# Kernel optimization log

Hardware: AMD Instinct MI355X
Metric: run time of the kernel (lower is better)

Reference implementation:

```python
import jax, jax.numpy as jnp
import numpy as np
import math

B, T, D = 1, 2048, 1024          # batch, seq, d_model
H, HS = 16, 64                    # heads, head_size
E, K, L = 8, 2, 2                 # experts, top_k, layers
V = 32000                         # llama tokenizer vocab
CAP = (B * T * K) // E            # expert capacity = 512
HALF = HS // 2


def _layernorm(x, w, b):
    m = jnp.mean(x, -1, keepdims=True)
    v = jnp.var(x, -1, keepdims=True)
    return (x - m) / jnp.sqrt(v + 1e-5) * w + b


def _rope_sincos():
    pos = jnp.arange(T, dtype=jnp.float32)[:, None]
    div = jnp.exp(jnp.arange(0, HALF * 2, 2, dtype=jnp.float32) * (-math.log(10000.0) / (HALF * 2)))
    return jnp.sin(pos * div), jnp.cos(pos * div)


def _attention(x, qkv_w, out_w, sin, cos):
    qkv = (x @ qkv_w.T).reshape(B, T, 3, H, HS)
    q, k, v = qkv[:, :, 0], qkv[:, :, 1], qkv[:, :, 2]
    s_, c_ = sin[None, :, None, :], cos[None, :, None, :]

    def rot(t):
        t1, t2 = t[..., :HALF], t[..., HALF:]
        return jnp.concatenate([t1 * c_ - t2 * s_, t2 * c_ + t1 * s_], -1)

    q, k = rot(q), rot(k)
    scores = jnp.einsum('bthd,bshd->bhts', q, k) / math.sqrt(HS)
    mask = jnp.tril(jnp.ones((T, T), bool))
    scores = jnp.where(mask[None, None], scores, -1e30)
    p = jax.nn.softmax(scores, -1)
    av = jnp.einsum('bhts,bshd->bthd', p, v)  # [B,T,H,HS]
    # faithful to torch source: permute(0,2,1,3).reshape(B,T,C)
    return av.transpose(0, 2, 1, 3).reshape(B, T, D) @ out_w.T


def _moe(x, noise_l, rw, rb, nw, nb, w1, b1, w2, b2):
    # NoisyTopkRouter + capacity-limited dispatch / expert MLP / weighted combine
    N = B * T
    xf = x.reshape(N, D)
    logits = xf @ rw.T + rb
    noisy = logits + noise_l.reshape(N, E) * jax.nn.softplus(xf @ nw.T + nb)
    topv, topi = jax.lax.top_k(noisy, K)
    # softmax over sparse logits (-inf elsewhere) == softmax over top-k values
    gate = jax.nn.softmax(topv, -1).reshape(-1)  # [N*K]
    ef = topi.reshape(-1)                        # expert id per (token,k) pair
    tid = jnp.repeat(jnp.arange(N), K)           # token id per pair
    oh = jax.nn.one_hot(ef, E, dtype=jnp.int32)
    # position of this token in its expert's arrival order (token-major, as nonzero())
    rank = (jnp.cumsum(oh, 0) - oh)[jnp.arange(N * K), ef]
    valid = rank < CAP
    pos = jnp.where(valid, ef * CAP + rank, E * CAP)  # dummy slot for dropped tokens
    disp = jnp.zeros((E * CAP + 1, D), x.dtype).at[pos].set(xf[tid])
    de = disp[:E * CAP].reshape(E, CAP, D)
    h = jax.nn.relu(jnp.einsum('ecd,efd->ecf', de, w1) + b1[:, None, :])
    eo = jnp.einsum('ecf,edf->ecd', h, w2) + b2[:, None, :]
    eo = jnp.concatenate([eo.reshape(E * CAP, D), jnp.zeros((1, D), x.dtype)], 0)
    contrib = eo[pos] * (gate * valid.astype(x.dtype))[:, None]
    return jax.ops.segment_sum(contrib, tid, num_segments=N).reshape(B, T, D)


def _forward(input_ids, noise, tok_emb, pos_emb, ln1_w, ln1_b, ln2_w, ln2_b,
             qkv_w, out_w, router_w, router_b, noise_w, noise_b,
             e_w1, e_b1, e_w2, e_b2, lnf_w, lnf_b):
    sin, cos = _rope_sincos()
    x = tok_emb[input_ids] + pos_emb[:T]
    for l in range(L):
        x = x + _attention(_layernorm(x, ln1_w[l], ln1_b[l]), qkv_w[l], out_w[l], sin, cos)
        x = x + _moe(_layernorm(x, ln2_w[l], ln2_b[l]), noise[l],
                     router_w[l], router_b[l], noise_w[l], noise_b[l],
                     e_w1[l], e_b1[l], e_w2[l], e_b2[l])
    return _layernorm(x, lnf_w, lnf_b)


def setup_inputs() -> dict:
    key = jax.random.key(0)
    ks = jax.random.split(key, 16)
    s = 0.02
    inp = {
        'input_ids': jax.random.randint(ks[0], (B, T), 0, V),
        'noise': jax.random.normal(ks[1], (L, B, T, E), jnp.float32),
        'tok_emb': jax.random.normal(ks[2], (V, D), jnp.float32) * s,
        'pos_emb': jax.random.normal(ks[3], (T, D), jnp.float32) * s,
        'ln1_w': jnp.ones((L, D), jnp.float32), 'ln1_b': jnp.zeros((L, D), jnp.float32),
        'ln2_w': jnp.ones((L, D), jnp.float32), 'ln2_b': jnp.zeros((L, D), jnp.float32),
        'qkv_w': jax.random.normal(ks[4], (L, 3 * D, D), jnp.float32) * s,
        'out_w': jax.random.normal(ks[5], (L, D, D), jnp.float32) * s,
        'router_w': jax.random.normal(ks[6], (L, E, D), jnp.float32) * s,
        'router_b': jnp.zeros((L, E), jnp.float32),
        'noise_w': jax.random.normal(ks[7], (L, E, D), jnp.float32) * s,
        'noise_b': jnp.zeros((L, E), jnp.float32),
        'e_w1': jax.random.normal(ks[8], (L, E, 4 * D, D), jnp.float32) * s,
        'e_b1': jnp.zeros((L, E, 4 * D), jnp.float32),
        'e_w2': jax.random.normal(ks[9], (L, E, D, 4 * D), jnp.float32) * s,
        'e_b2': jnp.zeros((L, E, D), jnp.float32),
        'lnf_w': jnp.ones((D,), jnp.float32), 'lnf_b': jnp.zeros((D,), jnp.float32),
    }
    return inp


def reference(input_ids, noise, tok_emb, pos_emb, ln1_w, ln1_b, ln2_w, ln2_b,
              qkv_w, out_w, router_w, router_b, noise_w, noise_b,
              e_w1, e_b1, e_w2, e_b2, lnf_w, lnf_b):
    return _forward(input_ids, noise, tok_emb, pos_emb, ln1_w, ln1_b, ln2_w, ln2_b,
                    qkv_w, out_w, router_w, router_b, noise_w, noise_b,
                    e_w1, e_b1, e_w2, e_b2, lnf_w, lnf_b)
```

## Files before the change

### kernel.cpp

```cpp
#include <hip/hip_runtime.h>
#include <math.h>

#define TT   2048
#define DD   1024
#define HH   16
#define HSS  64
#define EE   8
#define KTOP 2
#define LL   2
#define CAPP 512
#define NN   2048
#define DFF  4096
#define NK   (NN*KTOP)
#define HALF 32

typedef __attribute__((ext_vector_type(8))) short bf16x8;
typedef __attribute__((ext_vector_type(4))) float f32x4;

__device__ __forceinline__ void split3(float v, short& s0, short& s1, short& s2) {
  union { float f; unsigned u; } a, b0, c, b1, d;
  a.f = v;
  unsigned t0 = (a.u + 0x7fffu + ((a.u >> 16) & 1u)) & 0xffff0000u;
  b0.u = t0;
  float r1 = v - b0.f;
  c.f = r1;
  unsigned t1 = (c.u + 0x7fffu + ((c.u >> 16) & 1u)) & 0xffff0000u;
  b1.u = t1;
  float r2 = r1 - b1.f;
  d.f = r2;
  unsigned t2 = d.u + 0x7fffu + ((d.u >> 16) & 1u);
  s0 = (short)(t0 >> 16); s1 = (short)(t1 >> 16); s2 = (short)(t2 >> 16);
}

__device__ __forceinline__ void gld16(const short* g, short* l) {
  __builtin_amdgcn_global_load_lds(
      (const __attribute__((address_space(1))) unsigned int*)g,
      (__attribute__((address_space(3))) unsigned int*)l, 16, 0, 0);
}

__global__ __launch_bounds__(256) void embed_kernel(const int* __restrict__ ids,
                                                    const float* __restrict__ tok,
                                                    const float* __restrict__ pos,
                                                    float* __restrict__ x) {
  int t = blockIdx.x, tid = threadIdx.x;
  int id = ids[t];
  float4 a = ((const float4*)(tok + (long long)id * DD))[tid];
  float4 b = ((const float4*)(pos + (long long)t * DD))[tid];
  float4 r;
  r.x = a.x + b.x; r.y = a.y + b.y; r.z = a.z + b.z; r.w = a.w + b.w;
  ((float4*)(x + (long long)t * DD))[tid] = r;
}

__global__ __launch_bounds__(256) void sincos_kernel(float* __restrict__ st, float* __restrict__ ct) {
  int idx = blockIdx.x * 256 + threadIdx.x;
  int t = idx >> 5, i = idx & 31;
  double div = exp(-(double)(2 * i) * (9.210340371976184 / 64.0));
  double a = (double)t * div;
  st[idx] = (float)sin(a);
  ct[idx] = (float)cos(a);
}

__global__ __launch_bounds__(256) void convert_kernel(const float* __restrict__ in,
                                                      short* __restrict__ out, long long n) {
  long long i = ((long long)blockIdx.x * 256 + threadIdx.x) * 8;
  float4 v0 = *(const float4*)(in + i);
  float4 v1 = *(const float4*)(in + i + 4);
  float vv[8] = {v0.x, v0.y, v0.z, v0.w, v1.x, v1.y, v1.z, v1.w};
  short s0[8], s1[8], s2[8];
#pragma unroll
  for (int j = 0; j < 8; j++) split3(vv[j], s0[j], s1[j], s2[j]);
  *(short4*)(out + i)         = make_short4(s0[0], s0[1], s0[2], s0[3]);
  *(short4*)(out + i + 4)     = make_short4(s0[4], s0[5], s0[6], s0[7]);
  *(short4*)(out + n + i)     = make_short4(s1[0], s1[1], s1[2], s1[3]);
  *(short4*)(out + n + i + 4) = make_short4(s1[4], s1[5], s1[6], s1[7]);
  *(short4*)(out + 2*n + i)   = make_short4(s2[0], s2[1], s2[2], s2[3]);
  *(short4*)(out + 2*n + i+4) = make_short4(s2[4], s2[5], s2[6], s2[7]);
}

__global__ __launch_bounds__(256) void ln_kernel(const float* __restrict__ in, float* __restrict__ out,
                                                 short* __restrict__ yp,
                                                 const float* __restrict__ w, const float* __restrict__ b) {
  int row = blockIdx.x, tid = threadIdx.x;
  float4 v = ((const float4*)(in + (long long)row * DD))[tid];
  float s = v.x + v.y + v.z + v.w;
  float q = v.x * v.x + v.y * v.y + v.z * v.z + v.w * v.w;
#pragma unroll
  for (int off = 32; off > 0; off >>= 1) {
    s += __shfl_down(s, off);
    q += __shfl_down(q, off);
  }
  __shared__ float rs[4], rq[4];
  int wv = tid >> 6;
  if ((tid & 63) == 0) { rs[wv] = s; rq[wv] = q; }
  __syncthreads();
  float S = rs[0] + rs[1] + rs[2] + rs[3];
  float Q = rq[0] + rq[1] + rq[2] + rq[3];
  float mean = S * (1.0f / DD);
  float var = Q * (1.0f / DD) - mean * mean;
  float rstd = rsqrtf(var + 1e-5f);
  float4 wv4 = ((const float4*)w)[tid];
  float4 bv4 = ((const float4*)b)[tid];
  float4 r;
  r.x = (v.x - mean) * rstd * wv4.x + bv4.x;
  r.y = (v.y - mean) * rstd * wv4.y + bv4.y;
  r.z = (v.z - mean) * rstd * wv4.z + bv4.z;
  r.w = (v.w - mean) * rstd * wv4.w + bv4.w;
  ((float4*)(out + (long long)row * DD))[tid] = r;
  if (yp) {
    float rr[4] = {r.x, r.y, r.z, r.w};
    short a0[4], a1[4], a2[4];
#pragma unroll
    for (int j = 0; j < 4; j++) split3(rr[j], a0[j], a1[j], a2[j]);
    size_t off = (size_t)row * DD + tid * 4;
    *(short4*)(yp + off)                    = make_short4(a0[0], a0[1], a0[2], a0[3]);
    *(short4*)(yp + (size_t)NN*DD + off)    = make_short4(a1[0], a1[1], a1[2], a1[3]);
    *(short4*)(yp + (size_t)2*NN*DD + off)  = make_short4(a2[0], a2[1], a2[2], a2[3]);
  }
}

__global__ __launch_bounds__(256) void gemm_kernel(
    const float* __restrict__ Aall, const float* __restrict__ Ball,
    const float* __restrict__ biasAll, const float* __restrict__ resAll,
    float* __restrict__ Call, int M, int Nn, int Kd, int flags,
    long long sA, long long sB, long long sBias, long long sC) {
  const float* A = Aall + (long long)blockIdx.z * sA;
  const float* B = Ball + (long long)blockIdx.z * sB;
  float* C = Call + (long long)blockIdx.z * sC;
  __shared__ float As[128 * 17];
  __shared__ float Bs[128 * 17];
  int tid = threadIdx.x;
  int tx = tid & 15, ty = tid >> 4;
  int bm = blockIdx.y * 128, bn = blockIdx.x * 128;
  int lrow = tid >> 2;
  int lk = (tid & 3) << 2;
  float acc[8][8];
#pragma unroll
  for (int i = 0; i < 8; i++)
#pragma unroll
    for (int j = 0; j < 8; j++) acc[i][j] = 0.f;
  const float* Arow0 = A + (long long)(bm + lrow) * Kd + lk;
  const float* Arow1 = A + (long long)(bm + lrow + 64) * Kd + lk;
  const float* Brow0 = B + (long long)(bn + lrow) * Kd + lk;
  const float* Brow1 = B + (long long)(bn + lrow + 64) * Kd + lk;
  for (int kb = 0; kb < Kd; kb += 16) {
    float4 a0 = *(const float4*)(Arow0 + kb);
    float4 a1 = *(const float4*)(Arow1 + kb);
    float4 b0 = *(const float4*)(Brow0 + kb);
    float4 b1 = *(const float4*)(Brow1 + kb);
    __syncthreads();
    As[lrow * 17 + lk + 0] = a0.x; As[lrow * 17 + lk + 1] = a0.y;
    As[lrow * 17 + lk + 2] = a0.z; As[lrow * 17 + lk + 3] = a0.w;
    As[(lrow + 64) * 17 + lk + 0] = a1.x; As[(lrow + 64) * 17 + lk + 1] = a1.y;
    As[(lrow + 64) * 17 + lk + 2] = a1.z; As[(lrow + 64) * 17 + lk + 3] = a1.w;
    Bs[lrow * 17 + lk + 0] = b0.x; Bs[lrow * 17 + lk + 1] = b0.y;
    Bs[lrow * 17 + lk + 2] = b0.z; Bs[lrow * 17 + lk + 3] = b0.w;
    Bs[(lrow + 64) * 17 + lk + 0] = b1.x; Bs[(lrow + 64) * 17 + lk + 1] = b1.y;
    Bs[(lrow + 64) * 17 + lk + 2] = b1.z; Bs[(lrow + 64) * 17 + lk + 3] = b1.w;
    __syncthreads();
#pragma unroll
    for (int k = 0; k < 16; k++) {
      float av[8], bv[8];
#pragma unroll
      for (int i = 0; i < 8; i++) av[i] = As[(ty + 16 * i) * 17 + k];
#pragma unroll
      for (int j = 0; j < 8; j++) bv[j] = Bs[(tx + 16 * j) * 17 + k];
#pragma unroll
      for (int i = 0; i < 8; i++)
#pragma unroll
        for (int j = 0; j < 8; j++) acc[i][j] = fmaf(av[i], bv[j], acc[i][j]);
    }
  }
  const float* bias = (flags & 1) ? (biasAll + (long long)blockIdx.z * sBias) : nullptr;
  const float* res = (flags & 4) ? (resAll + (long long)blockIdx.z * sC) : nullptr;
#pragma unroll
  for (int i = 0; i < 8; i++) {
    int row = bm + ty + 16 * i;
#pragma unroll
    for (int j = 0; j < 8; j++) {
      int col = bn + tx + 16 * j;
      float v = acc[i][j];
      if (flags & 1) v += bias[col];
      if (flags & 2) v = fmaxf(v, 0.f);
      if (flags & 4) v += res[(long long)row * Nn + col];
      C[(long long)row * Nn + col] = v;
    }
  }
}

__global__ __launch_bounds__(256, 3) void gemm_mfma(
    const short* __restrict__ Ap, const short* __restrict__ Bp,
    const float* __restrict__ biasAll, const float* __restrict__ resAll,
    void* __restrict__ Call, int M, int Nn, int Kd, int flags,
    long long sA, long long sB, long long sBias, long long sC,
    long long PA, long long PB, long long PC) {
  const bool fast = (flags & 8);
  const int np = fast ? 2 : 3;
  const int splitK = (flags >> 8) & 0xff;
  __shared__ short As[3][128][32];
  __shared__ short Bs[3][128][32];
  int tid = threadIdx.x;

  int gx = gridDim.x, gy = gridDim.y;
  int nwg = gx * gy * gridDim.z;
  int flat = blockIdx.x + gx * (blockIdx.y + gy * blockIdx.z);
  int cpx = nwg >> 3;
  int wkid = (flat & 7) * cpx + (flat >> 3);
  int bz = wkid / (gx * gy);
  int rem = wkid - bz * gx * gy;
  int by = rem / gx, bx = rem - by * gx;

  int sk = 0, e = bz, kLen = Kd;
  if (splitK > 1) { sk = bz % splitK; e = bz / splitK; kLen = Kd / splitK; }
  int k0 = sk * kLen;

  int bm = by * 128, bn = bx * 128;
  long long zA = (long long)e * sA;
  long long zB = (long long)e * sB;

  int wid = tid >> 6, lane = tid & 63;
  int lrow = lane >> 2, lchunk = lane & 3;
  int cs = lchunk ^ ((lrow >> 1) & 3);
  const short* gAbase = Ap + zA + (long long)(bm + wid * 16 + lrow) * Kd + cs * 8;
  const short* gBbase = Bp + zB + (long long)(bn + wid * 16 + lrow) * Kd + cs * 8;
  long long hstepA = (long long)64 * Kd;

  int wm = (wid & 1) * 64, wn = (wid >> 1) * 64;
  int tr = lane & 15, quad = lane >> 4;
  int qsw = (quad ^ ((tr >> 1) & 3)) << 3;

  f32x4 acc[4][4];
#pragma unroll
  for (int i = 0; i < 4; i++)
#pragma unroll
    for (int j = 0; j < 4; j++) acc[i][j] = (f32x4){0.f, 0.f, 0.f, 0.f};

  for (int kb = k0; kb < k0 + kLen; kb += 32) {
    __syncthreads();
#pragma unroll
    for (int p = 0; p < 3; p++) {
      if (p < np) {
#pragma unroll
        for (int h = 0; h < 2; h++) {
          int rb = h * 64 + wid * 16;
          gld16(gAbase + p * PA + h * hstepA + kb, &As[p][rb][0]);
          gld16(gBbase + p * PB + h * hstepA + kb, &Bs[p][rb][0]);
        }
      }
    }
    __syncthreads();
    bf16x8 af[4][3];
#pragma unroll
    for (int mi = 0; mi < 4; mi++) {
      int ar = wm + mi * 16 + tr;
      af[mi][0] = *(const bf16x8*)&As[0][ar][qsw];
      af[mi][1] = *(const bf16x8*)&As[1][ar][qsw];
      af[mi][2] = fast ? af[mi][0] : *(const bf16x8*)&As[2][ar][qsw];
    }
#pragma unroll
    for (int nj = 0; nj < 4; nj++) {
      int br = wn + nj * 16 + tr;
      bf16x8 b0 = *(const bf16x8*)&Bs[0][br][qsw];
      bf16x8 b1 = *(const bf16x8*)&Bs[1][br][qsw];
      bf16x8 b2 = fast ? b0 : *(const bf16x8*)&Bs[2][br][qsw];
#pragma unroll
      for (int mi = 0; mi < 4; mi++) {
        f32x4 c = acc[mi][nj];
        c = __builtin_amdgcn_mfma_f32_16x16x32_bf16(af[mi][1], b0, c, 0, 0, 0);
        c = __builtin_amdgcn_mfma_f32_16x16x32_bf16(af[mi][0], b1, c, 0, 0, 0);
        if (!fast) {
          c = __builtin_amdgcn_mfma_f32_16x16x32_bf16(af[mi][2], b0, c, 0, 0, 0);
          c = __builtin_amdgcn_mfma_f32_16x16x32_bf16(af[mi][1], b1, c, 0, 0, 0);
          c = __builtin_amdgcn_mfma_f32_16x16x32_bf16(af[mi][0], b2, c, 0, 0, 0);
        }
        c = __builtin_amdgcn_mfma_f32_16x16x32_bf16(af[mi][0], b0, c, 0, 0, 0);
        acc[mi][nj] = c;
      }
    }
  }

  long long z = e;
  if (splitK > 1) {
    int NB = nwg / (gx * gy) / splitK;
    float* P = (float*)Call;
    long long base = ((long long)sk * NB + e) * sC;
#pragma unroll
    for (int mi = 0; mi < 4; mi++)
#pragma unroll
      for (int nj = 0; nj < 4; nj++) {
        int col = bn + wn + nj * 16 + tr;
#pragma unroll
        for (int rg = 0; rg < 4; rg++) {
          int row = bm + wm + mi * 16 + quad * 4 + rg;
          P[base + (long long)row * Nn + col] = acc[mi][nj][rg];
        }
      }
    return;
  }
  const float* bias = (flags & 1) ? (biasAll + z * sBias) : nullptr;
  if (flags & 16) {
    short* Cs = (short*)Call;
#pragma unroll
    for (int mi = 0; mi < 4; mi++)
#pragma unroll
      for (int nj = 0; nj < 4; nj++) {
        int col = bn + wn + nj * 16 + tr;
#pragma unroll
        for (int rg = 0; rg < 4; rg++) {
          int row = bm + wm + mi * 16 + quad * 4 + rg;
          float v = acc[mi][nj][rg];
          if (flags & 1) v += bias[col];
          if (flags & 2) v = fmaxf(v, 0.f);
          short s0, s1, s2;
          split3(v, s0, s1, s2);
          long long off = z * sC + (long long)row * Nn + col;
          Cs[off] = s0; Cs[PC + off] = s1; Cs[2 * PC + off] = s2;
        }
      }
  } else {
    float* C = (float*)Call;
    const float* res = (flags & 4) ? (resAll + z * sC) : nullptr;
#pragma unroll
    for (int mi = 0; mi < 4; mi++)
#pragma unroll
      for (int nj = 0; nj < 4; nj++) {
        int col = bn + wn + nj * 16 + tr;
#pragma unroll
        for (int rg = 0; rg < 4; rg++) {
          int row = bm + wm + mi * 16 + quad * 4 + rg;
          float v = acc[mi][nj][rg];
          if (flags & 1) v += bias[col];
          if (flags & 2) v = fmaxf(v, 0.f);
          if (flags & 4) v += res[(long long)row * Nn + col];
          C[z * sC + (long long)row * Nn + col] = v;
        }
      }
  }
  (void)M;
}

__global__ __launch_bounds__(256) void reduce_kernel(
    float* __restrict__ dst, const float* __restrict__ part,
    const float* __restrict__ biasAll, int splits, long long total,
    int Nn, long long MNn, long long sBias, int flags) {
  long long i = ((long long)blockIdx.x * 256 + threadIdx.x) * 4;
  if (i >= total) return;
  float4 v = make_float4(0.f, 0.f, 0.f, 0.f);
  for (int s = 0; s < splits; s++) {
    float4 p = *(const float4*)(part + (long long)s * total + i);
    v.x += p.x; v.y += p.y; v.z += p.z; v.w += p.w;
  }
  if (flags & 1) {
    long long e = i / MNn;
    int col = (int)(i % Nn);
    const float* b = biasAll + e * sBias + col;
    v.x += b[0]; v.y += b[1]; v.z += b[2]; v.w += b[3];
  }
  if (flags & 4) {
    float4 r = *(const float4*)(dst + i);
    v.x += r.x; v.y += r.y; v.z += r.z; v.w += r.w;
  }
  *(float4*)(dst + i) = v;
}

__global__ __launch_bounds__(256) void rope_kernel(float* __restrict__ qkv,
                                                   const float* __restrict__ st,
                                                   const float* __restrict__ ct) {
  int t = blockIdx.x, tid = threadIdx.x;
#pragma unroll
  for (int p = tid; p < HH * HALF; p += 256) {
    int h = p >> 5, i = p & 31;
    float s = st[t * HALF + i], c = ct[t * HALF + i];
    float* q = qkv + (long long)t * (3 * DD) + h * HSS;
    float q1 = q[i], q2 = q[i + HALF];
    q[i] = q1 * c - q2 * s;
    q[i + HALF] = q2 * c + q1 * s;
    float* k = q + DD;
    float k1 = k[i], k2 = k[i + HALF];
    k[i] = k1 * c - k2 * s;
    k[i + HALF] = k2 * c + k1 * s;
  }
}

__global__ __launch_bounds__(256, 1) void attn_kernel(const float* __restrict__ qkv,
                                                      float* __restrict__ attn,
                                                      short* __restrict__ ap) {
  int bid = blockIdx.x;
  int head = bid & 15;
  int qc = (bid < 256) ? (31 - (bid >> 4)) : ((bid - 256) >> 4);
  int tid = threadIdx.x;
  int w = tid >> 6;
  int r = tid & 63;
  int qrow = qc * 64 + r;
  int nkt = qc + 1;

  __shared__ float4 KVbuf[4][2][16][16];
  __shared__ float Ms[4][64];
  __shared__ float Ls[4][64];

  float4 q[16], o[16];
  const float4* qp = (const float4*)(qkv + (long long)qrow * (3 * DD) + head * HSS);
#pragma unroll
  for (int d = 0; d < 16; d++) { q[d] = qp[d]; o[d] = make_float4(0.f, 0.f, 0.f, 0.f); }
  float m = -INFINITY, l = 0.f;

  for (int kt = w; kt < nkt; kt += 4) {
    bool diag = (kt == qc);
#pragma unroll 1
    for (int s = 0; s < 4; s++) {
      int kbase = kt * 64 + s * 16;
#pragma unroll
      for (int it = 0; it < 4; it++) {
        int fid = r + it * 64;
        int krow = fid >> 4, d4 = fid & 15;
        const float* bK = qkv + (long long)(kbase + krow) * (3 * DD) + DD + head * HSS + d4 * 4;
        KVbuf[w][0][krow][d4] = *(const float4*)bK;
        KVbuf[w][1][krow][d4] = *(const float4*)(bK + DD);
      }
      float sbuf[16];
#pragma unroll
      for (int jj = 0; jj < 16; jj++) {
        const float4* kr = KVbuf[w][0][jj];
        float sv = 0.f;
#pragma unroll
        for (int d = 0; d < 16; d++) {
          float4 kv = kr[d];
          sv = fmaf(q[d].x, kv.x, sv); sv = fmaf(q[d].y, kv.y, sv);
          sv = fmaf(q[d].z, kv.z, sv); sv = fmaf(q[d].w, kv.w, sv);
        }
        sv *= 0.125f;
        if (diag && (kbase + jj > qrow)) sv = -1e30f;
        sbuf[jj] = sv;
      }
      float gm = m;
#pragma unroll
      for (int jj = 0; jj < 16; jj++) gm = fmaxf(gm, sbuf[jj]);
      float scale = __expf(m - gm);
      m = gm;
      l *= scale;
#pragma unroll
      for (int d = 0; d < 16; d++) {
        o[d].x *= scale; o[d].y *= scale; o[d].z *= scale; o[d].w *= scale;
      }
#pragma unroll
      for (int jj = 0; jj < 16; jj++) {
        float p = __expf(sbuf[jj] - m);
        l += p;
        const float4* vr = KVbuf[w][1][jj];
#pragma unroll
        for (int d = 0; d < 16; d++) {
          float4 vv = vr[d];
          o[d].x = fmaf(p, vv.x, o[d].x); o[d].y = fmaf(p, vv.y, o[d].y);
          o[d].z = fmaf(p, vv.z, o[d].z); o[d].w = fmaf(p, vv.w, o[d].w);
        }
      }
    }
  }

  typedef float4 OscRow[64][5];
  OscRow* Osc = reinterpret_cast<OscRow*>(&KVbuf[0][0][0][0]);
  int rr = tid & 63, ii = tid >> 6;
  long long obase = (long long)head * TT * HSS + (long long)(qc * 64 + rr) * HSS;
#pragma unroll
  for (int c = 0; c < 4; c++) {
    __syncthreads();
    Osc[w][r][0] = o[c * 4 + 0];
    Osc[w][r][1] = o[c * 4 + 1];
    Osc[w][r][2] = o[c * 4 + 2];
    Osc[w][r][3] = o[c * 4 + 3];
    if (c == 0) { Ms[w][r] = m; Ls[w][r] = l; }
    __syncthreads();
    float m0 = Ms[0][rr], m1 = Ms[1][rr], m2 = Ms[2][rr], m3 = Ms[3][rr];
    float M = fmaxf(fmaxf(m0, m1), fmaxf(m2, m3));
    float s0 = __expf(m0 - M), s1 = __expf(m1 - M);
    float s2 = __expf(m2 - M), s3 = __expf(m3 - M);
    float L = s0 * Ls[0][rr] + s1 * Ls[1][rr] + s2 * Ls[2][rr] + s3 * Ls[3][rr];
    float rl = 1.f / L;
    float4 a0 = Osc[0][rr][ii], a1 = Osc[1][rr][ii];
    float4 a2 = Osc[2][rr][ii], a3 = Osc[3][rr][ii];
    float4 res;
    res.x = (s0 * a0.x + s1 * a1.x + s2 * a2.x + s3 * a3.x) * rl;
    res.y = (s0 * a0.y + s1 * a1.y + s2 * a2.y + s3 * a3.y) * rl;
    res.z = (s0 * a0.z + s1 * a1.z + s2 * a2.z + s3 * a3.z) * rl;
    res.w = (s0 * a0.w + s1 * a1.w + s2 * a2.w + s3 * a3.w) * rl;
    long long oaddr = obase + c * 16 + ii * 4;
    *(float4*)(attn + oaddr) = res;
    if (ap) {
      float rv[4] = {res.x, res.y, res.z, res.w};
      short p0[4], p1[4], p2[4];
#pragma unroll
      for (int j = 0; j < 4; j++) split3(rv[j], p0[j], p1[j], p2[j]);
      *(short4*)(ap + oaddr)                    = make_short4(p0[0], p0[1], p0[2], p0[3]);
      *(short4*)(ap + (size_t)NN*DD + oaddr)    = make_short4(p1[0], p1[1], p1[2], p1[3]);
      *(short4*)(ap + (size_t)2*NN*DD + oaddr)  = make_short4(p2[0], p2[1], p2[2], p2[3]);
    }
  }
}

__global__ __launch_bounds__(64) void router_kernel(
    const float* __restrict__ y, const float* __restrict__ rw, const float* __restrict__ rb,
    const float* __restrict__ nw, const float* __restrict__ nb, const float* __restrict__ noise,
    int* __restrict__ slot_e, float* __restrict__ slot_g) {
  int n = blockIdx.x;
  int lane = threadIdx.x;
  double accr[EE], accn[EE];
#pragma unroll
  for (int e = 0; e < EE; e++) { accr[e] = 0.0; accn[e] = 0.0; }
  for (int j = 0; j < 16; j++) {
    float xv = y[(long long)n * DD + j * 64 + lane];
#pragma unroll
    for (int e = 0; e < EE; e++) {
      accr[e] += (double)xv * (double)rw[e * DD + j * 64 + lane];
      accn[e] += (double)xv * (double)nw[e * DD + j * 64 + lane];
    }
  }
#pragma unroll
  for (int e = 0; e < EE; e++) {
    for (int off = 32; off > 0; off >>= 1) {
      accr[e] += __shfl_down(accr[e], off);
      accn[e] += __shfl_down(accn[e], off);
    }
  }
  if (lane == 0) {
    float noisy[EE];
#pragma unroll
    for (int e = 0; e < EE; e++) {
      float lg = (float)accr[e] + rb[e];
      float nl = (float)accn[e] + nb[e];
      float sp = (nl > 0.f) ? (nl + log1pf(expf(-nl))) : log1pf(expf(nl));
      noisy[e] = lg + noise[n * EE + e] * sp;
    }
    int i0 = 0;
#pragma unroll
    for (int e = 1; e < EE; e++) if (noisy[e] > noisy[i0]) i0 = e;
    int i1 = -1;
#pragma unroll
    for (int e = 0; e < EE; e++) {
      if (e == i0) continue;
      if (i1 < 0 || noisy[e] > noisy[i1]) i1 = e;
    }
    float v0 = noisy[i0], v1 = noisy[i1];
    float e1 = __expf(v1 - v0);
    float inv = 1.f / (1.f + e1);
    slot_e[2 * n] = i0; slot_e[2 * n + 1] = i1;
    slot_g[2 * n] = inv; slot_g[2 * n + 1] = e1 * inv;
  }
}

__global__ __launch_bounds__(256) void scan_kernel(const int* __restrict__ slot_e,
                                                   int* __restrict__ slot_pos) {
  __shared__ int cnt[256 * EE];
  int tid = threadIdx.x;
  int base = tid * 16;
  int c[EE];
#pragma unroll
  for (int e = 0; e < EE; e++) c[e] = 0;
  int loc[16];
  for (int i = 0; i < 16; i++) {
    int e = slot_e[base + i];
    loc[i] = e;
    c[e]++;
  }
#pragma unroll
  for (int e = 0; e < EE; e++) cnt[tid * EE + e] = c[e];
  __syncthreads();
  if (tid < EE) {
    int run = 0;
    for (int t2 = 0; t2 < 256; t2++) {
      int v = cnt[t2 * EE + tid];
      cnt[t2 * EE + tid] = run;
      run += v;
    }
  }
  __syncthreads();
  int run[EE];
#pragma unroll
  for (int e = 0; e < EE; e++) run[e] = cnt[tid * EE + e];
  for (int i = 0; i < 16; i++) {
    int e = loc[i];
    int r = run[e]++;
    slot_pos[base + i] = (r < CAPP) ? (e * CAPP + r) : -1;
  }
}

__global__ __launch_bounds__(256) void dispatch_kernel(const float* __restrict__ y,
                                                       const int* __restrict__ slot_pos,
                                                       float* __restrict__ disp) {
  int i = blockIdx.x;
  int pos = slot_pos[i];
  if (pos < 0) return;
  int tok = i >> 1;
  ((float4*)(disp + (long long)pos * DD))[threadIdx.x] =
      ((const float4*)(y + (long long)tok * DD))[threadIdx.x];
}

__global__ __launch_bounds__(256) void dispatch_planes_kernel(const short* __restrict__ yp,
                                                              const int* __restrict__ slot_pos,
                                                              short* __restrict__ dp) {
  int i = blockIdx.x;
  int pos = slot_pos[i];
  if (pos < 0) return;
  int tok = i >> 1;
#pragma unroll
  for (int p = 0; p < 3; p++) {
    short4 v = ((const short4*)(yp + (size_t)p * NN * DD + (size_t)tok * DD))[threadIdx.x];
    ((short4*)(dp + (size_t)p * EE * CAPP * DD + (size_t)pos * DD))[threadIdx.x] = v;
  }
}

__global__ __launch_bounds__(256) void combine_kernel(float* __restrict__ x,
                                                      const float* __restrict__ eo,
                                                      const int* __restrict__ slot_pos,
                                                      const float* __restrict__ slot_g) {
  int n = blockIdx.x, tid = threadIdx.x;
  int p0 = slot_pos[2 * n], p1 = slot_pos[2 * n + 1];
  float g0 = slot_g[2 * n], g1 = slot_g[2 * n + 1];
  float4 v = ((float4*)(x + (long long)n * DD))[tid];
  if (p0 >= 0) {
    float4 e0 = ((const float4*)(eo + (long long)p0 * DD))[tid];
    v.x = fmaf(g0, e0.x, v.x); v.y = fmaf(g0, e0.y, v.y);
    v.z = fmaf(g0, e0.z, v.z); v.w = fmaf(g0, e0.w, v.w);
  }
  if (p1 >= 0) {
    float4 e1 = ((const float4*)(eo + (long long)p1 * DD))[tid];
    v.x = fmaf(g1, e1.x, v.x); v.y = fmaf(g1, e1.y, v.y);
    v.z = fmaf(g1, e1.z, v.z); v.w = fmaf(g1, e1.w, v.w);
  }
  ((float4*)(x + (long long)n * DD))[tid] = v;
}

extern "C" void kernel_launch(void* const* d_in, const int* in_sizes, int n_in,
                              void* d_out, int out_size, void* d_ws, size_t ws_size,
                              hipStream_t stream) {
  const int* input_ids = (const int*)d_in[0];
  const float* noise = (const float*)d_in[1];
  const float* tok_emb = (const float*)d_in[2];
  const float* pos_emb = (const float*)d_in[3];
  const float* ln1_w = (const float*)d_in[4];
  const float* ln1_b = (const float*)d_in[5];
  const float* ln2_w = (const float*)d_in[6];
  const float* ln2_b = (const float*)d_in[7];
  const float* qkv_w = (const float*)d_in[8];
  const float* out_w = (const float*)d_in[9];
  const float* router_w = (const float*)d_in[10];
  const float* router_b = (const float*)d_in[11];
  const float* noise_w = (const float*)d_in[12];
  const float* noise_b = (const float*)d_in[13];
  const float* e_w1 = (const float*)d_in[14];
  const float* e_b1 = (const float*)d_in[15];
  const float* e_w2 = (const float*)d_in[16];
  const float* e_b2 = (const float*)d_in[17];
  const float* lnf_w = (const float*)d_in[18];
  const float* lnf_b = (const float*)d_in[19];
  float* out = (float*)d_out;

  float* ws = (float*)d_ws;
  size_t off = 0;
  float* x = ws + off;       off += (size_t)NN * DD;
  float* y = ws + off;       off += (size_t)NN * DD;
  float* qkv = ws + off;     off += (size_t)NN * 3 * DD;
  float* eo = ws + off;      off += (size_t)EE * CAPP * DD;
  float* sintab = ws + off;  off += (size_t)TT * HALF;
  float* costab = ws + off;  off += (size_t)TT * HALF;
  float* attn32 = ws + off;  off += (size_t)NN * DD;
  int* slot_e = (int*)(ws + off);   off += NK;
  int* slot_pos = (int*)(ws + off); off += NK;
  float* slot_g = ws + off;  off += NK;
  size_t base_floats = off;
  float* disp32 = ws + off;
  float* hbuf32 = disp32 + (size_t)EE * CAPP * DD;
  size_t fb_need = (base_floats + (size_t)EE * CAPP * DD + (size_t)EE * CAPP * DFF) * 4;

  short* sp = (short*)(ws + base_floats);
  short* y_p = sp;                                   sp += (size_t)3 * NN * DD;
  short* attn_p = sp;                                sp += (size_t)3 * NN * DD;
  short* disp_p = sp;                                sp += (size_t)3 * EE * CAPP * DD;
  short* hbuf_p = sp;                                sp += (size_t)3 * EE * CAPP * DFF;
  short* qkvw_p = sp;                                sp += (size_t)3 * LL * 3 * DD * DD;
  short* outw_p = sp;                                sp += (size_t)3 * LL * DD * DD;
  short* ew_p = sp;                                  sp += (size_t)3 * EE * DFF * DD;
  size_t mfma_need = (size_t)((char*)sp - (char*)d_ws);
  bool use_mfma = (ws_size >= mfma_need);
  (void)fb_need;

  float* pQKV = (float*)hbuf_p;
  float* pAO  = (float*)hbuf_p;
  float* pM2  = y;

  embed_kernel<<<TT, 256, 0, stream>>>(input_ids, tok_emb, pos_emb, x);
  sincos_kernel<<<(TT * HALF) / 256, 256, 0, stream>>>(sintab, costab);

  if (use_mfma) {
    long long nq = (long long)LL * 3 * DD * DD;
    long long no = (long long)LL * DD * DD;
    convert_kernel<<<(int)(nq / 2048), 256, 0, stream>>>(qkv_w, qkvw_p, nq);
    convert_kernel<<<(int)(no / 2048), 256, 0, stream>>>(out_w, outw_p, no);
    long long ne = (long long)EE * DFF * DD;

    for (int l = 0; l < LL; l++) {
      int fastf = (l == LL - 1) ? 8 : 0;
      ln_kernel<<<NN, 256, 0, stream>>>(x, y, y_p, ln1_w + l * DD, ln1_b + l * DD);
      gemm_mfma<<<dim3(3 * DD / 128, NN / 128, 2), 256, 0, stream>>>(
          y_p, qkvw_p + (size_t)l * 3 * DD * DD, nullptr, nullptr, pQKV,
          NN, 3 * DD, DD, (2 << 8), 0, 0, 0, (long long)NN * 3 * DD,
          (long long)NN * DD, (long long)LL * 3 * DD * DD, 0);
      reduce_kernel<<<(int)((long long)NN * 3 * DD / 1024), 256, 0, stream>>>(
          qkv, pQKV, nullptr, 2, (long long)NN * 3 * DD, 3 * DD,
          (long long)NN * 3 * DD, 0, 0);
      rope_kernel<<<TT, 256, 0, stream>>>(qkv, sintab, costab);
      attn_kernel<<<512, 256, 0, stream>>>(qkv, attn32, attn_p);
      gemm_mfma<<<dim3(DD / 128, NN / 128, 4), 256, 0, stream>>>(
          attn_p, outw_p + (size_t)l * DD * DD, nullptr, nullptr, pAO,
          NN, DD, DD, (4 << 8), 0, 0, 0, (long long)NN * DD,
          (long long)NN * DD, (long long)LL * DD * DD, 0);
      reduce_kernel<<<(int)((long long)NN * DD / 1024), 256, 0, stream>>>(
          x, pAO, nullptr, 4, (long long)NN * DD, DD, (long long)NN * DD, 0, 4);
      ln_kernel<<<NN, 256, 0, stream>>>(x, y, y_p, ln2_w + l * DD, ln2_b + l * DD);
      router_kernel<<<NN, 64, 0, stream>>>(
          y, router_w + (size_t)l * EE * DD, router_b + l * EE,
          noise_w + (size_t)l * EE * DD, noise_b + l * EE,
          noise + (size_t)l * NN * EE, slot_e, slot_g);
      scan_kernel<<<1, 256, 0, stream>>>(slot_e, slot_pos);
      dispatch_planes_kernel<<<NK, 256, 0, stream>>>(y_p, slot_pos, disp_p);
      convert_kernel<<<(int)(ne / 2048), 256, 0, stream>>>(e_w1 + (size_t)l * ne, ew_p, ne);
      gemm_mfma<<<dim3(DFF / 128, CAPP / 128, EE), 256, 0, stream>>>(
          disp_p, ew_p, e_b1 + (size_t)l * EE * DFF, nullptr, hbuf_p,
          CAPP, DFF, DD, 1 | 2 | 16 | fastf,
          (long long)CAPP * DD, (long long)DFF * DD, DFF, (long long)CAPP * DFF,
          (long long)EE * CAPP * DD, (long long)EE * DFF * DD, (long long)EE * CAPP * DFF);
      convert_kernel<<<(int)(ne / 2048), 256, 0, stream>>>(e_w2 + (size_t)l * ne, ew_p, ne);
      gemm_mfma<<<dim3(DD / 128, CAPP / 128, EE * 2), 256, 0, stream>>>(
          hbuf_p, ew_p, nullptr, nullptr, pM2,
          CAPP, DD, DFF, fastf | (2 << 8),
          (long long)CAPP * DFF, (long long)DD * DFF, 0, (long long)CAPP * DD,
          (long long)EE * CAPP * DFF, (long long)EE * DD * DFF, 0);
      reduce_kernel<<<(int)((long long)EE * CAPP * DD / 1024), 256, 0, stream>>>(
          eo, pM2, e_b2 + (size_t)l * EE * DD, 2, (long long)EE * CAPP * DD, DD,
          (long long)CAPP * DD, DD, 1);
      combine_kernel<<<NN, 256, 0, stream>>>(x, eo, slot_pos, slot_g);
    }
  } else {
    for (int l = 0; l < LL; l++) {
      ln_kernel<<<NN, 256, 0, stream>>>(x, y, nullptr, ln1_w + l * DD, ln1_b + l * DD);
      gemm_kernel<<<dim3(3 * DD / 128, NN / 128, 1), 256, 0, stream>>>(
          y, qkv_w + (size_t)l * 3 * DD * DD, nullptr, nullptr, qkv,
          NN, 3 * DD, DD, 0, 0, 0, 0, 0);
      rope_kernel<<<TT, 256, 0, stream>>>(qkv, sintab, costab);
      attn_kernel<<<512, 256, 0, stream>>>(qkv, attn32, nullptr);
      gemm_kernel<<<dim3(DD / 128, NN / 128, 1), 256, 0, stream>>>(
          attn32, out_w + (size_t)l * DD * DD, nullptr, x, x,
          NN, DD, DD, 4, 0, 0, 0, 0);
      ln_kernel<<<NN, 256, 0, stream>>>(x, y, nullptr, ln2_w + l * DD, ln2_b + l * DD);
      router_kernel<<<NN, 64, 0, stream>>>(
          y, router_w + (size_t)l * EE * DD, router_b + l * EE,
          noise_w + (size_t)l * EE * DD, noise_b + l * EE,
          noise + (size_t)l * NN * EE, slot_e, slot_g);
      scan_kernel<<<1, 256, 0, stream>>>(slot_e, slot_pos);
      dispatch_kernel<<<NK, 256, 0, stream>>>(y, slot_pos, disp32);
      gemm_kernel<<<dim3(DFF / 128, CAPP / 128, EE), 256, 0, stream>>>(
          disp32, e_w1 + (size_t)l * EE * DFF * DD, e_b1 + (size_t)l * EE * DFF, nullptr, hbuf32,
          CAPP, DFF, DD, 3,
          (long long)CAPP * DD, (long long)DFF * DD, DFF, (long long)CAPP * DFF);
      gemm_kernel<<<dim3(DD / 128, CAPP / 128, EE), 256, 0, stream>>>(
          hbuf32, e_w2 + (size_t)l * EE * DD * DFF, e_b2 + (size_t)l * EE * DD, nullptr, eo,
          CAPP, DD, DFF, 1,
          (long long)CAPP * DFF, (long long)DD * DFF, DD, (long long)CAPP * DD);
      combine_kernel<<<NN, 256, 0, stream>>>(x, eo, slot_pos, slot_g);
    }
  }
  ln_kernel<<<NN, 256, 0, stream>>>(x, out, nullptr, lnf_w, lnf_b);
  (void)in_sizes; (void)n_in; (void)out_size; (void)ws_size;
}
```

Baseline: 2.559 ms.

## Move causal attention onto bf16 MFMA with split-precision Q/K/V planes

Replaces the fp32 scalar flash-attention kernel with an MFMA-based kernel that uses 3-term bf16 split products (hi*hi, hi*lo, lo*hi) for QK^T and PV. Two new prep kernels fuse RoPE into producing hi/lo bf16 planes for Q and K and write a transposed V in hi/lo planes, staged in LDS through swizzled global_load_lds. The goal is to cut the attention compute cost by using matrix cores, at the price of extra prep passes, workspace traffic and slightly reduced precision versus full fp32.

```diff
diff --git a/kernel.cpp b/kernel.cpp
--- a/kernel.cpp
+++ b/kernel.cpp
@@ -30,6 +30,17 @@
   d.f = r2;
   unsigned t2 = d.u + 0x7fffu + ((d.u >> 16) & 1u);
   s0 = (short)(t0 >> 16); s1 = (short)(t1 >> 16); s2 = (short)(t2 >> 16);
+}
+
+__device__ __forceinline__ void split2(float v, short& s0, short& s1) {
+  union { float f; unsigned u; } a, b0, c;
+  a.f = v;
+  unsigned t0 = (a.u + 0x7fffu + ((a.u >> 16) & 1u)) & 0xffff0000u;
+  b0.u = t0;
+  float r1 = v - b0.f;
+  c.f = r1;
+  unsigned t1 = c.u + 0x7fffu + ((c.u >> 16) & 1u);
+  s0 = (short)(t0 >> 16); s1 = (short)(t1 >> 16);
 }
 
 __device__ __forceinline__ void gld16(const short* g, short* l) {
@@ -381,6 +392,223 @@
   }
 }
 
+__global__ __launch_bounds__(256) void qk_rope_planes_kernel(
+    const float* __restrict__ qkv, const float* __restrict__ st, const float* __restrict__ ct,
+    short* __restrict__ Qp, short* __restrict__ Kp) {
+  int h = blockIdx.x >> 5, tb = blockIdx.x & 31;
+  int tid = threadIdx.x;
+  int d0 = (tid & 7) * 4;
+#pragma unroll
+  for (int pp = 0; pp < 2; pp++) {
+    int t = tb * 64 + pp * 32 + (tid >> 3);
+    const float* row = qkv + (size_t)t * (3 * DD) + h * HSS;
+    float4 qa = *(const float4*)(row + d0);
+    float4 qb = *(const float4*)(row + d0 + HALF);
+    float4 ka = *(const float4*)(row + DD + d0);
+    float4 kb = *(const float4*)(row + DD + d0 + HALF);
+    float4 s4 = *(const float4*)(st + (size_t)t * HALF + d0);
+    float4 c4 = *(const float4*)(ct + (size_t)t * HALF + d0);
+    float qa_[4] = {qa.x, qa.y, qa.z, qa.w}, qb_[4] = {qb.x, qb.y, qb.z, qb.w};
+    float ka_[4] = {ka.x, ka.y, ka.z, ka.w}, kb_[4] = {kb.x, kb.y, kb.z, kb.w};
+    float ss[4] = {s4.x, s4.y, s4.z, s4.w}, cc[4] = {c4.x, c4.y, c4.z, c4.w};
+    short qh0[4], ql0[4], qh1[4], ql1[4];
+    short kh0[4], kl0[4], kh1[4], kl1[4];
+#pragma unroll
+    for (int u = 0; u < 4; u++) {
+      float o1 = qa_[u] * cc[u] - qb_[u] * ss[u];
+      float o2 = qb_[u] * cc[u] + qa_[u] * ss[u];
+      split2(o1, qh0[u], ql0[u]);
+      split2(o2, qh1[u], ql1[u]);
+      float p1 = ka_[u] * cc[u] - kb_[u] * ss[u];
+      float p2 = kb_[u] * cc[u] + ka_[u] * ss[u];
+      split2(p1, kh0[u], kl0[u]);
+      split2(p2, kh1[u], kl1[u]);
+    }
+    size_t b0 = ((size_t)(h * 2 + 0) * TT + t) * 64 + d0;
+    size_t b1 = ((size_t)(h * 2 + 1) * TT + t) * 64 + d0;
+    *(short4*)(Qp + b0)        = make_short4(qh0[0], qh0[1], qh0[2], qh0[3]);
+    *(short4*)(Qp + b0 + HALF) = make_short4(qh1[0], qh1[1], qh1[2], qh1[3]);
+    *(short4*)(Qp + b1)        = make_short4(ql0[0], ql0[1], ql0[2], ql0[3]);
+    *(short4*)(Qp + b1 + HALF) = make_short4(ql1[0], ql1[1], ql1[2], ql1[3]);
+    *(short4*)(Kp + b0)        = make_short4(kh0[0], kh0[1], kh0[2], kh0[3]);
+    *(short4*)(Kp + b0 + HALF) = make_short4(kh1[0], kh1[1], kh1[2], kh1[3]);
+    *(short4*)(Kp + b1)        = make_short4(kl0[0], kl0[1], kl0[2], kl0[3]);
+    *(short4*)(Kp + b1 + HALF) = make_short4(kl1[0], kl1[1], kl1[2], kl1[3]);
+  }
+}
+
+__global__ __launch_bounds__(256) void v_planes_kernel(const float* __restrict__ qkv,
+                                                       short* __restrict__ Vt) {
+  int h = blockIdx.x >> 5, tb = blockIdx.x & 31;
+  int tid = threadIdx.x;
+  __shared__ float Vsl[64][65];
+#pragma unroll
+  for (int pp = 0; pp < 4; pp++) {
+    int r = pp * 16 + (tid >> 4);
+    int d0 = (tid & 15) * 4;
+    float4 v = *(const float4*)(qkv + (size_t)(tb * 64 + r) * (3 * DD) + 2 * DD + h * HSS + d0);
+    Vsl[r][d0] = v.x; Vsl[r][d0 + 1] = v.y; Vsl[r][d0 + 2] = v.z; Vsl[r][d0 + 3] = v.w;
+  }
+  __syncthreads();
+  int d = tid >> 2, tq = tid & 3;
+  short hs[16], lsv[16];
+#pragma unroll
+  for (int jj = 0; jj < 16; jj++) split2(Vsl[tq * 16 + jj][d], hs[jj], lsv[jj]);
+  size_t b0 = ((size_t)(h * 2 + 0) * 64 + d) * TT + tb * 64 + tq * 16;
+  size_t b1 = ((size_t)(h * 2 + 1) * 64 + d) * TT + tb * 64 + tq * 16;
+#pragma unroll
+  for (int g = 0; g < 4; g++) {
+    *(short4*)(Vt + b0 + g * 4) = make_short4(hs[g*4], hs[g*4+1], hs[g*4+2], hs[g*4+3]);
+    *(short4*)(Vt + b1 + g * 4) = make_short4(lsv[g*4], lsv[g*4+1], lsv[g*4+2], lsv[g*4+3]);
+  }
+}
+
+__global__ __launch_bounds__(256, 3) void attn_mfma_kernel(
+    const short* __restrict__ Qp, const short* __restrict__ Kp,
+    const short* __restrict__ Vt, short* __restrict__ ap) {
+  int bid = blockIdx.x;
+  int head = bid & 15;
+  int qc = (bid < 256) ? (31 - (bid >> 4)) : ((bid - 256) >> 4);
+  int tid = threadIdx.x;
+  int w = tid >> 6, lane = tid & 63;
+  int tr = lane & 15, quad = lane >> 4;
+  int lr = lane >> 3, lc = lane & 7;
+
+  __shared__ short Ks[2][64][64];
+  __shared__ short Vs[2][64][64];
+  __shared__ short Ps[4][2][16][64];
+
+  bf16x8 qf[2][2];
+  int qrow = qc * 64 + w * 16 + tr;
+#pragma unroll
+  for (int kk = 0; kk < 2; kk++)
+#pragma unroll
+    for (int p = 0; p < 2; p++)
+      qf[kk][p] = *(const bf16x8*)(Qp + ((size_t)(head * 2 + p) * TT + qrow) * 64 + kk * 32 + quad * 8);
+
+  f32x4 acc_o[4];
+#pragma unroll
+  for (int nj = 0; nj < 4; nj++) acc_o[nj] = (f32x4){0.f, 0.f, 0.f, 0.f};
+  float m = -INFINITY, l = 0.f;
+
+  int nkt = qc + 1;
+  for (int kt = 0; kt < nkt; kt++) {
+    __syncthreads();
+#pragma unroll
+    for (int p = 0; p < 2; p++)
+#pragma unroll
+      for (int h = 0; h < 2; h++) {
+        int r = h * 32 + w * 8 + lr;
+        gld16(Kp + ((size_t)(head * 2 + p) * TT + kt * 64 + r) * 64 + (lc ^ (r & 7)) * 8,
+              &Ks[p][h * 32 + w * 8][0]);
+        gld16(Vt + ((size_t)(head * 2 + p) * 64 + r) * TT + kt * 64 + (lc ^ (r & 7)) * 8,
+              &Vs[p][h * 32 + w * 8][0]);
+      }
+    __syncthreads();
+
+    f32x4 sc[4];
+#pragma unroll
+    for (int mi = 0; mi < 4; mi++) {
+      f32x4 s = (f32x4){0.f, 0.f, 0.f, 0.f};
+      int kr = mi * 16 + tr;
+#pragma unroll
+      for (int kk = 0; kk < 2; kk++) {
+        int cidx = ((kk * 4 + quad) ^ (kr & 7)) * 8;
+        bf16x8 k0 = *(const bf16x8*)&Ks[0][kr][cidx];
+        bf16x8 k1 = *(const bf16x8*)&Ks[1][kr][cidx];
+        s = __builtin_amdgcn_mfma_f32_16x16x32_bf16(k1, qf[kk][0], s, 0, 0, 0);
+        s = __builtin_amdgcn_mfma_f32_16x16x32_bf16(k0, qf[kk][1], s, 0, 0, 0);
+        s = __builtin_amdgcn_mfma_f32_16x16x32_bf16(k0, qf[kk][0], s, 0, 0, 0);
+      }
+      sc[mi] = s;
+    }
+    bool diag = (kt == qc);
+    float pmax = -INFINITY;
+#pragma unroll
+    for (int mi = 0; mi < 4; mi++)
+#pragma unroll
+      for (int rg = 0; rg < 4; rg++) {
+        float v = sc[mi][rg] * 0.125f;
+        if (diag && (mi * 16 + quad * 4 + rg > w * 16 + tr)) v = -1e30f;
+        sc[mi][rg] = v;
+        pmax = fmaxf(pmax, v);
+      }
+    pmax = fmaxf(pmax, __shfl_xor(pmax, 16));
+    pmax = fmaxf(pmax, __shfl_xor(pmax, 32));
+    float mnew = fmaxf(m, pmax);
+    float scl = __expf(m - mnew);
+    m = mnew;
+    float ps = 0.f;
+#pragma unroll
+    for (int mi = 0; mi < 4; mi++)
+#pragma unroll
+      for (int rg = 0; rg < 4; rg++) {
+        float p = __expf(sc[mi][rg] - mnew);
+        sc[mi][rg] = p;
+        ps += p;
+      }
+    ps += __shfl_xor(ps, 16);
+    ps += __shfl_xor(ps, 32);
+    l = l * scl + ps;
+#pragma unroll
+    for (int mi = 0; mi < 4; mi++) {
+      short h0, h1, h2, h3, l0, l1, l2, l3;
+      split2(sc[mi][0], h0, l0); split2(sc[mi][1], h1, l1);
+      split2(sc[mi][2], h2, l2); split2(sc[mi][3], h3, l3);
+      int off8 = ((mi * 4 + quad) ^ ((tr & 7) << 1)) * 4;
+      *(short4*)&Ps[w][0][tr][off8] = make_short4(h0, h1, h2, h3);
+      *(short4*)&Ps[w][1][tr][off8] = make_short4(l0, l1, l2, l3);
+    }
+    asm volatile("s_waitcnt lgkmcnt(0)" ::: "memory");
+    float srg[4];
+#pragma unroll
+    for (int rg = 0; rg < 4; rg++) srg[rg] = __shfl(scl, quad * 4 + rg);
+#pragma unroll
+    for (int nj = 0; nj < 4; nj++)
+#pragma unroll
+      for (int rg = 0; rg < 4; rg++) acc_o[nj][rg] *= srg[rg];
+    bf16x8 pf[2][2];
+#pragma unroll
+    for (int ks = 0; ks < 2; ks++)
+#pragma unroll
+      for (int pl = 0; pl < 2; pl++)
+        pf[ks][pl] = *(const bf16x8*)&Ps[w][pl][tr][((ks * 4 + quad) ^ (tr & 7)) * 8];
+#pragma unroll
+    for (int nj = 0; nj < 4; nj++) {
+      f32x4 o = acc_o[nj];
+      int vr = nj * 16 + tr;
+#pragma unroll
+      for (int ks = 0; ks < 2; ks++) {
+        int cidx = ((ks * 4 + quad) ^ (vr & 7)) * 8;
+        bf16x8 v0 = *(const bf16x8*)&Vs[0][vr][cidx];
+        bf16x8 v1 = *(const bf16x8*)&Vs[1][vr][cidx];
+        o = __builtin_amdgcn_mfma_f32_16x16x32_bf16(pf[ks][1], v0, o, 0, 0, 0);
+        o = __builtin_amdgcn_mfma_f32_16x16x32_bf16(pf[ks][0], v1, o, 0, 0, 0);
+        o = __builtin_amdgcn_mfma_f32_16x16x32_bf16(pf[ks][0], v0, o, 0, 0, 0);
+      }
+      acc_o[nj] = o;
+    }
+  }
+
+  float rl[4];
+#pragma unroll
+  for (int rg = 0; rg < 4; rg++) rl[rg] = 1.f / __shfl(l, quad * 4 + rg);
+#pragma unroll
+  for (int nj = 0; nj < 4; nj++)
+#pragma unroll
+    for (int rg = 0; rg < 4; rg++) {
+      float v = acc_o[nj][rg] * rl[rg];
+      int q = qc * 64 + w * 16 + quad * 4 + rg;
+      int d = nj * 16 + tr;
+      size_t oaddr = (size_t)head * TT * HSS + (size_t)q * HSS + d;
+      short s0, s1, s2;
+      split3(v, s0, s1, s2);
+      ap[oaddr] = s0;
+      ap[(size_t)NN * DD + oaddr] = s1;
+      ap[(size_t)2 * NN * DD + oaddr] = s2;
+    }
+}
+
 __global__ __launch_bounds__(256, 1) void attn_kernel(const float* __restrict__ qkv,
                                                       float* __restrict__ attn,
                                                       short* __restrict__ ap) {
@@ -474,14 +702,14 @@
     float s0 = __expf(m0 - M), s1 = __expf(m1 - M);
     float s2 = __expf(m2 - M), s3 = __expf(m3 - M);
     float L = s0 * Ls[0][rr] + s1 * Ls[1][rr] + s2 * Ls[2][rr] + s3 * Ls[3][rr];
-    float rl = 1.f / L;
+    float rlq = 1.f / L;
     float4 a0 = Osc[0][rr][ii], a1 = Osc[1][rr][ii];
     float4 a2 = Osc[2][rr][ii], a3 = Osc[3][rr][ii];
     float4 res;
-    res.x = (s0 * a0.x + s1 * a1.x + s2 * a2.x + s3 * a3.x) * rl;
-    res.y = (s0 * a0.y + s1 * a1.y + s2 * a2.y + s3 * a3.y) * rl;
-    res.z = (s0 * a0.z + s1 * a1.z + s2 * a2.z + s3 * a3.z) * rl;
-    res.w = (s0 * a0.w + s1 * a1.w + s2 * a2.w + s3 * a3.w) * rl;
+    res.x = (s0 * a0.x + s1 * a1.x + s2 * a2.x + s3 * a3.x) * rlq;
+    res.y = (s0 * a0.y + s1 * a1.y + s2 * a2.y + s3 * a3.y) * rlq;
+    res.z = (s0 * a0.z + s1 * a1.z + s2 * a2.z + s3 * a3.z) * rlq;
+    res.w = (s0 * a0.w + s1 * a1.w + s2 * a2.w + s3 * a3.w) * rlq;
     long long oaddr = obase + c * 16 + ii * 4;
     *(float4*)(attn + oaddr) = res;
     if (ap) {
@@ -685,6 +913,9 @@
   float* pQKV = (float*)hbuf_p;
   float* pAO  = (float*)hbuf_p;
   float* pM2  = y;
+  short* attnQp = hbuf_p;
+  short* attnKp = attnQp + (size_t)HH * 2 * TT * HSS;
+  short* attnVt = attnKp + (size_t)HH * 2 * TT * HSS;
 
   embed_kernel<<<TT, 256, 0, stream>>>(input_ids, tok_emb, pos_emb, x);
   sincos_kernel<<<(TT * HALF) / 256, 256, 0, stream>>>(sintab, costab);
@@ -706,8 +937,9 @@
       reduce_kernel<<<(int)((long long)NN * 3 * DD / 1024), 256, 0, stream>>>(
           qkv, pQKV, nullptr, 2, (long long)NN * 3 * DD, 3 * DD,
           (long long)NN * 3 * DD, 0, 0);
-      rope_kernel<<<TT, 256, 0, stream>>>(qkv, sintab, costab);
-      attn_kernel<<<512, 256, 0, stream>>>(qkv, attn32, attn_p);
+      qk_rope_planes_kernel<<<512, 256, 0, stream>>>(qkv, sintab, costab, attnQp, attnKp);
+      v_planes_kernel<<<512, 256, 0, stream>>>(qkv, attnVt);
+      attn_mfma_kernel<<<512, 256, 0, stream>>>(attnQp, attnKp, attnVt, attn_p);
       gemm_mfma<<<dim3(DD / 128, NN / 128, 4), 256, 0, stream>>>(
           attn_p, outw_p + (size_t)l * DD * DD, nullptr, nullptr, pAO,
           NN, DD, DD, (4 << 8), 0, 0, 0, (long long)NN * DD,
```

Result: faster. 2.058 ms (-19.6%).
